# Performance work log

Measured on AMD Instinct MI355X. Metric: run time of the kernel, lower is better.

The kernel has to match this reference:

```python
import jax, jax.numpy as jnp
import numpy as np

E = 512
H = 8
DH = E // H
LN_EPS = 1e-5


def setup_inputs() -> dict:
    key = jax.random.key(0)
    ks = jax.random.split(key, 8)
    s = 1.0 / np.sqrt(E)
    return {
        "query": jax.random.normal(ks[0], (2, 2048, E), jnp.float32),
        "key_value": jax.random.normal(ks[1], (2, 4096, E), jnp.float32),
        "Wq": jax.random.normal(ks[2], (E, E), jnp.float32) * s,
        "bq": jnp.zeros((E,), jnp.float32),
        "Wk": jax.random.normal(ks[3], (E, E), jnp.float32) * s,
        "bk": jnp.zeros((E,), jnp.float32),
        "Wv": jax.random.normal(ks[4], (E, E), jnp.float32) * s,
        "bv": jnp.zeros((E,), jnp.float32),
        "Wo": jax.random.normal(ks[5], (E, E), jnp.float32) * s,
        "bo": jnp.zeros((E,), jnp.float32),
        "ln_gamma": jnp.ones((E,), jnp.float32),
        "ln_beta": jnp.zeros((E,), jnp.float32),
    }


def reference(query, key_value, Wq, bq, Wk, bk, Wv, bv, Wo, bo, ln_gamma, ln_beta):
    B, Lq, _ = query.shape
    Lk = key_value.shape[1]
    # Projections (torch Linear: x @ W.T + b)
    q = (query @ Wq.T + bq).reshape(B, Lq, H, DH)
    k = (key_value @ Wk.T + bk).reshape(B, Lk, H, DH)
    v = (key_value @ Wv.T + bv).reshape(B, Lk, H, DH)
    scale = 1.0 / np.sqrt(DH).astype(np.float32)
    scores = jnp.einsum("bqhd,bkhd->bhqk", q, k) * scale  # [B,H,Lq,Lk]
    attn = jax.nn.softmax(scores, axis=-1)
    ctx = jnp.einsum("bhqk,bkhd->bqhd", attn, v).reshape(B, Lq, E)
    attn_out = ctx @ Wo.T + bo
    # residual + LayerNorm (dropout is identity in eval)
    x = query + attn_out
    mu = jnp.mean(x, axis=-1, keepdims=True)
    var = jnp.mean(jnp.square(x - mu), axis=-1, keepdims=True)
    return (x - mu) * jax.lax.rsqrt(var + LN_EPS) * ln_gamma + ln_beta
```

## Files before the change

### kernel.cpp

```cpp
#include <hip/hip_runtime.h>
#include <hip/hip_bf16.h>

typedef __bf16 bf16;
typedef __bf16 bf16x8 __attribute__((ext_vector_type(8)));
typedef __bf16 bf16x4 __attribute__((ext_vector_type(4)));
typedef float f32x4 __attribute__((ext_vector_type(4)));

#define MFMA16(a, b, c) __builtin_amdgcn_mfma_f32_16x16x32_bf16((a), (b), (c), 0, 0, 0)

constexpr int LQ = 2048, LK = 4096, E = 512, H = 8, DH = 64;
#define QSCALE 0.1803368801111137f

#if __has_builtin(__builtin_amdgcn_exp2f)
#define EXP2(x) __builtin_amdgcn_exp2f(x)
#else
#define EXP2(x) __expf(0.6931471805599453f * (x))
#endif

__device__ __forceinline__ bf16x8 ld8(const bf16* p) { return *(const bf16x8*)p; }

__global__ __launch_bounds__(256) void cvt4_kernel(
    const float* __restrict__ w0, const float* __restrict__ w1,
    const float* __restrict__ w2, const float* __restrict__ w3,
    bf16* __restrict__ dst) {
  const float* srcs[4] = {w0, w1, w2, w3};
  const float* src = srcs[blockIdx.y];
  bf16* d = dst + (size_t)blockIdx.y * 262144;
  int i = (blockIdx.x * 256 + threadIdx.x) * 4;
  f32x4 v = *(const f32x4*)(src + i);
  bf16x4 o;
  for (int j = 0; j < 4; ++j) o[j] = (bf16)v[j];
  *(bf16x4*)(d + i) = o;
}

__global__ __launch_bounds__(256) void proj_gemm_kernel(
    const float* __restrict__ query, const float* __restrict__ kv,
    const bf16* __restrict__ Wall,
    const float* __restrict__ bq, const float* __restrict__ bk,
    const float* __restrict__ bv,
    bf16* __restrict__ qproj, bf16* __restrict__ kproj, bf16* __restrict__ vt) {
  __shared__ bf16 smA[2][128][72];
  __shared__ bf16 smB[2][128][72];
  const int tid = threadIdx.x;
  const int lane = tid & 63, wave = tid >> 6;
  const int lrow = lane & 15, quad = lane >> 4;
  const int wm = wave & 1, wn = wave >> 1;

  int x = blockIdx.x, z, mt;
  if (x < 32) { z = 0; mt = x; }
  else if (x < 96) { z = 1; mt = x - 32; }
  else { z = 2; mt = x - 96; }
  const float* A = ((z == 0) ? query : kv) + (size_t)mt * 128 * E;
  const bf16* W = Wall + (size_t)z * 262144;
  const float* bias = (z == 0) ? bq : (z == 1) ? bk : bv;
  const int n0 = blockIdx.y * 128;

  const int arow = tid >> 4, acol = tid & 15;
  const int brow = tid >> 3, bcol = tid & 7;

  f32x4 pa[8];
  bf16x8 pb[4];
#define LOAD_T(t)                                                             \
  {                                                                           \
    for (int p = 0; p < 8; ++p)                                               \
      pa[p] = *(const f32x4*)(A + (size_t)(p * 16 + arow) * E + (t) * 64 +    \
                              acol * 4);                                      \
    for (int p = 0; p < 4; ++p)                                               \
      pb[p] = ld8(W + (size_t)(n0 + p * 32 + brow) * E + (t) * 64 + bcol * 8);\
  }
#define STORE_T(bs)                                                           \
  {                                                                           \
    for (int p = 0; p < 8; ++p) {                                             \
      bf16x4 av;                                                              \
      for (int e = 0; e < 4; ++e) av[e] = (bf16)pa[p][e];                     \
      *(bf16x4*)&smA[bs][p * 16 + arow][acol * 4] = av;                       \
    }                                                                         \
    for (int p = 0; p < 4; ++p)                                               \
      *(bf16x8*)&smB[bs][p * 32 + brow][bcol * 8] = pb[p];                    \
  }

  LOAD_T(0);
  STORE_T(0);
  LOAD_T(1);
  __syncthreads();

  f32x4 acc[4][4] = {};
  for (int t = 0; t < 8; ++t) {
    const int bs = t & 1;
    bf16x8 af[2][4], bfr[2][4];
    for (int ks = 0; ks < 2; ++ks)
      for (int i = 0; i < 4; ++i)
        af[ks][i] = ld8(&smA[bs][wm * 64 + 16 * i + lrow][ks * 32 + quad * 8]);
    for (int ks = 0; ks < 2; ++ks)
      for (int c = 0; c < 4; ++c)
        bfr[ks][c] = ld8(&smB[bs][wn * 64 + 16 * c + lrow][ks * 32 + quad * 8]);
    for (int ks = 0; ks < 2; ++ks)
      for (int i = 0; i < 4; ++i)
        for (int c = 0; c < 4; ++c)
          acc[i][c] = MFMA16(af[ks][i], bfr[ks][c], acc[i][c]);
    if (t < 7) {
      STORE_T(bs ^ 1);
      if (t < 6) LOAD_T(t + 2);
    }
    __syncthreads();
  }
#undef LOAD_T
#undef STORE_T

  const float qsc = (z == 0) ? QSCALE : 1.f;
  float bvl[4];
  for (int c = 0; c < 4; ++c) bvl[c] = bias[n0 + wn * 64 + 16 * c + lrow];
  bf16* Cs = &smA[0][0][0];
  for (int i = 0; i < 4; ++i)
    for (int c = 0; c < 4; ++c)
      for (int r = 0; r < 4; ++r) {
        int row = wm * 64 + 16 * i + 4 * quad + r;
        int col = wn * 64 + 16 * c + lrow;
        bf16 val = (bf16)((acc[i][c][r] + bvl[c]) * qsc);
        if (z < 2) Cs[row * 136 + col] = val;
        else       Cs[col * 136 + row] = val;
      }
  __syncthreads();
  const int rr = tid >> 1, hh = tid & 1;
  if (z < 2) {
    bf16* Y = (z == 0) ? qproj : kproj;
    bf16* dstp = Y + (size_t)(mt * 128 + rr) * E + n0 + hh * 64;
    for (int j = 0; j < 8; ++j)
      *(bf16x8*)(dstp + j * 8) = *(bf16x8*)&Cs[rr * 136 + hh * 64 + j * 8];
  } else {
    int m0g = mt * 128, b = m0g >> 12, kk0 = m0g & 4095;
    int ng = n0 + rr, hd = ng >> 6, d = ng & 63;
    bf16* dstp = vt + ((size_t)((b * 8 + hd) * 64 + d)) * LK + kk0 + hh * 64;
    for (int j = 0; j < 8; ++j)
      *(bf16x8*)(dstp + j * 8) = *(bf16x8*)&Cs[rr * 136 + hh * 64 + j * 8];
  }
}

__global__ __launch_bounds__(256, 2) void attn_kernel(
    const bf16* __restrict__ qp, const bf16* __restrict__ kp,
    const bf16* __restrict__ vtg, bf16* __restrict__ ctx) {
  const int tid = threadIdx.x;
  const int lane = tid & 63, wave = tid >> 6;
  const int lrow = lane & 15, quad = lane >> 4;
  const int blk = blockIdx.x;
  const int qt = blk & 31, bh = blk >> 5;
  const int b = bh >> 3, h = bh & 7;
  const int wq = wave & 1, half = wave >> 1;
  const int q0 = qt * 64 + wq * 32;

  __shared__ bf16 Ks[2][2][32][72];
  __shared__ bf16 Vs[2][2][64][40];
  __shared__ bf16 Ps[4][32][40];
  __shared__ float Lr[2][2][16];

  bf16x8 qf[2][2];
  for (int g = 0; g < 2; ++g)
    for (int s = 0; s < 2; ++s)
      qf[g][s] = ld8(qp + (size_t)(b * LQ + q0 + 16 * g + lrow) * E + h * DH +
                     32 * s + quad * 8);

  float lrun[2] = {0.f, 0.f};
  f32x4 acc[2][4] = {};

  const int th = tid & 127;
  const int krow = th >> 2, kch = th & 3;
  const int vrow = th >> 1, vch = th & 1;
  const bf16* kbase =
      kp + ((size_t)(b * LK) + half * 2048 + krow) * E + h * DH + kch * 16;
  const bf16* vbase =
      vtg + ((size_t)bh * DH + vrow) * LK + half * 2048 + vch * 16;

  bf16x8 pk0 = ld8(kbase), pk1 = ld8(kbase + 8);
  bf16x8 pv0 = ld8(vbase), pv1 = ld8(vbase + 8);

  for (int it = 0; it < 64; ++it) {
    const int bs = it & 1;
    *(bf16x8*)&Ks[half][bs][krow][kch * 16] = pk0;
    *(bf16x8*)&Ks[half][bs][krow][kch * 16 + 8] = pk1;
    *(bf16x8*)&Vs[half][bs][vrow][vch * 16] = pv0;
    *(bf16x8*)&Vs[half][bs][vrow][vch * 16 + 8] = pv1;
    __syncthreads();

    if (it < 63) {
      const bf16* kn = kbase + (size_t)(it + 1) * 32 * E;
      const bf16* vn = vbase + (it + 1) * 32;
      pk0 = ld8(kn); pk1 = ld8(kn + 8);
      pv0 = ld8(vn); pv1 = ld8(vn + 8);
    }

    bf16x8 kf[2][2], vf[4];
    for (int kt = 0; kt < 2; ++kt)
      for (int sd = 0; sd < 2; ++sd)
        kf[kt][sd] = ld8(&Ks[half][bs][16 * kt + lrow][32 * sd + quad * 8]);
    for (int c = 0; c < 4; ++c)
      vf[c] = ld8(&Vs[half][bs][16 * c + lrow][quad * 8]);

    f32x4 st[2][2];
    for (int g = 0; g < 2; ++g)
      for (int kt = 0; kt < 2; ++kt) {
        st[g][kt] = (f32x4){0.f, 0.f, 0.f, 0.f};
        st[g][kt] = MFMA16(kf[kt][0], qf[g][0], st[g][kt]);
        st[g][kt] = MFMA16(kf[kt][1], qf[g][1], st[g][kt]);
      }
    for (int g = 0; g < 2; ++g)
      for (int kt = 0; kt < 2; ++kt) {
        bf16x4 pp;
        for (int r = 0; r < 4; ++r) {
          float p = EXP2(st[g][kt][r]);
          lrun[g] += p;
          pp[r] = (bf16)p;
        }
        *(bf16x4*)&Ps[wave][16 * g + lrow][16 * kt + 4 * quad] = pp;
      }
    for (int g = 0; g < 2; ++g) {
      bf16x8 pf = ld8(&Ps[wave][16 * g + lrow][quad * 8]);
      for (int c = 0; c < 4; ++c)
        acc[g][c] = MFMA16(pf, vf[c], acc[g][c]);
    }
  }

  for (int g = 0; g < 2; ++g) {
    lrun[g] += __shfl_xor(lrun[g], 16);
    lrun[g] += __shfl_xor(lrun[g], 32);
  }

  __syncthreads();
  float* F = (float*)&Ks[0][0][0][0];
  if (half == 1) {
    for (int g = 0; g < 2; ++g)
      for (int c = 0; c < 4; ++c)
        for (int r = 0; r < 4; ++r)
          F[(wq * 32 + 16 * g + 4 * quad + r) * 65 + 16 * c + lrow] =
              acc[g][c][r];
    if (lane < 16)
      for (int g = 0; g < 2; ++g) Lr[wq][g][lrow] = lrun[g];
  }
  __syncthreads();
  if (half == 0) {
    for (int g = 0; g < 2; ++g)
      for (int r = 0; r < 4; ++r) {
        float l0 = __shfl(lrun[g], 4 * quad + r);
        float l1 = Lr[wq][g][4 * quad + r];
        float inv = 1.f / (l0 + l1);
        int m = q0 + 16 * g + 4 * quad + r;
        bf16* dst = ctx + (size_t)(b * LQ + m) * E + h * DH;
        for (int c = 0; c < 4; ++c) {
          float o = acc[g][c][r] +
                    F[(wq * 32 + 16 * g + 4 * quad + r) * 65 + 16 * c + lrow];
          dst[16 * c + lrow] = (bf16)(o * inv);
        }
      }
  }
}

__global__ __launch_bounds__(512) void outln_kernel(
    const bf16* __restrict__ Cx, const bf16* __restrict__ Wo,
    const float* __restrict__ bo, const float* __restrict__ resid,
    const float* __restrict__ gamma, const float* __restrict__ beta,
    float* __restrict__ out) {
  const int tid = threadIdx.x;
  const int lane = tid & 63, wave = tid >> 6;
  const int lrow = lane & 15, quad = lane >> 4;
  const int m0 = blockIdx.x * 16;
  const int n0 = wave * 64;

  __shared__ bf16 As[16][520];
  __shared__ bf16 Wos[512][72];
  __shared__ float red1[16][8], red2[16][8];
  {
    int r = tid >> 5, ch = tid & 31;
    const bf16* src = Cx + (size_t)(m0 + r) * E + ch * 16;
    *(bf16x8*)&As[r][ch * 16] = ld8(src);
    *(bf16x8*)&As[r][ch * 16 + 8] = ld8(src + 8);
  }
  const int wr = tid >> 3, wc = tid & 7;
  bf16x8 pw[8];
  for (int p = 0; p < 8; ++p)
    pw[p] = ld8(Wo + (size_t)(p * 64 + wr) * E + wc * 8);
  __syncthreads();

  f32x4 acc[4] = {};
  for (int t = 0; t < 8; ++t) {
    for (int p = 0; p < 8; ++p)
      *(bf16x8*)&Wos[p * 64 + wr][wc * 8] = pw[p];
    __syncthreads();
    if (t < 7)
      for (int p = 0; p < 8; ++p)
        pw[p] = ld8(Wo + (size_t)(p * 64 + wr) * E + (t + 1) * 64 + wc * 8);
    for (int ks = 0; ks < 2; ++ks) {
      bf16x8 a = *(const bf16x8*)&As[lrow][t * 64 + ks * 32 + quad * 8];
      for (int c = 0; c < 4; ++c) {
        bf16x8 w = *(const bf16x8*)&Wos[n0 + 16 * c + lrow][ks * 32 + quad * 8];
        acc[c] = MFMA16(a, w, acc[c]);
      }
    }
    __syncthreads();
  }

  float s1[4] = {}, s2[4] = {};
  for (int c = 0; c < 4; ++c) {
    int n = n0 + 16 * c + lrow;
    float bb = bo[n];
    for (int r = 0; r < 4; ++r) {
      int m = 4 * quad + r;
      float xv = acc[c][r] + bb + resid[(size_t)(m0 + m) * E + n];
      acc[c][r] = xv;
      s1[r] += xv;
      s2[r] += xv * xv;
    }
  }
  for (int off = 1; off < 16; off <<= 1)
    for (int r = 0; r < 4; ++r) {
      s1[r] += __shfl_xor(s1[r], off);
      s2[r] += __shfl_xor(s2[r], off);
    }
  if (lrow == 0)
    for (int r = 0; r < 4; ++r) {
      red1[4 * quad + r][wave] = s1[r];
      red2[4 * quad + r][wave] = s2[r];
    }
  __syncthreads();
  float mu[4], rstd[4];
  for (int r = 0; r < 4; ++r) {
    int m = 4 * quad + r;
    float t1 = 0.f, t2 = 0.f;
    for (int w = 0; w < 8; ++w) { t1 += red1[m][w]; t2 += red2[m][w]; }
    float mean = t1 * (1.f / 512.f);
    float var = t2 * (1.f / 512.f) - mean * mean;
    mu[r] = mean;
    rstd[r] = rsqrtf(var + 1e-5f);
  }
  for (int c = 0; c < 4; ++c) {
    int n = n0 + 16 * c + lrow;
    float gm = gamma[n], bt = beta[n];
    for (int r = 0; r < 4; ++r) {
      int m = m0 + 4 * quad + r;
      out[(size_t)m * E + n] = (acc[c][r] - mu[r]) * rstd[r] * gm + bt;
    }
  }
}

extern "C" void kernel_launch(void* const* d_in, const int* in_sizes, int n_in,
                              void* d_out, int out_size, void* d_ws, size_t ws_size,
                              hipStream_t stream) {
  const float* query     = (const float*)d_in[0];
  const float* key_value = (const float*)d_in[1];
  const float* Wq = (const float*)d_in[2];
  const float* bq = (const float*)d_in[3];
  const float* Wk = (const float*)d_in[4];
  const float* bk = (const float*)d_in[5];
  const float* Wv = (const float*)d_in[6];
  const float* bv = (const float*)d_in[7];
  const float* Wo = (const float*)d_in[8];
  const float* bo = (const float*)d_in[9];
  const float* gamma = (const float*)d_in[10];
  const float* beta  = (const float*)d_in[11];
  float* out = (float*)d_out;

  bf16* Wb    = (bf16*)d_ws;
  bf16* Wob   = Wb + (size_t)3 * 262144;
  bf16* qproj = Wb + (size_t)4 * 262144;
  bf16* kproj = qproj + (size_t)4096 * 512;
  bf16* vt    = kproj + (size_t)8192 * 512;

  cvt4_kernel<<<dim3(256, 4), 256, 0, stream>>>(Wq, Wk, Wv, Wo, Wb);
  proj_gemm_kernel<<<dim3(160, 4), 256, 0, stream>>>(
      query, key_value, Wb, bq, bk, bv, qproj, kproj, vt);
  attn_kernel<<<512, 256, 0, stream>>>(qproj, kproj, vt, qproj );
  outln_kernel<<<256, 512, 0, stream>>>(qproj, Wob, bo, query, gamma, beta, out);
}
```

Measured before the change: 188.1 us.

## Split attention keys four ways per block, reading K/V fragments directly from global

The attention kernel now gives each of its four waves a quarter of the key sequence for a 32-query tile, doubling the grid and raising launch bounds to 4 blocks per SM. The LDS staging and per-iteration barriers for K/V are removed, and MFMA fragments are loaded straight from global/L2. Block indices are swizzled so that co-resident blocks share heads, and s_setprio is wrapped around the MFMA sections. A four-way LDS reduction merges the partial outputs and row sums. The aim is to drop barrier and LDS overhead and raise occupancy, at the cost of more uncoalesced global loads and more redundant K/V traffic across blocks.

Result: slower. 246.1 us (+30.8%).

```diff
diff --git a/kernel.cpp b/kernel.cpp
--- a/kernel.cpp
+++ b/kernel.cpp
@@ -136,22 +136,24 @@
   }
 }
 
-__global__ __launch_bounds__(256, 2) void attn_kernel(
+__global__ __launch_bounds__(256, 4) void attn_kernel(
     const bf16* __restrict__ qp, const bf16* __restrict__ kp,
     const bf16* __restrict__ vtg, bf16* __restrict__ ctx) {
   const int tid = threadIdx.x;
   const int lane = tid & 63, wave = tid >> 6;
   const int lrow = lane & 15, quad = lane >> 4;
-  const int blk = blockIdx.x;
-  const int qt = blk & 31, bh = blk >> 5;
+  const int hw = blockIdx.x;
+  const int blk = (hw & 7) * 128 + (hw >> 3);
+  const int bh = blk >> 6, qt = blk & 63;
   const int b = bh >> 3, h = bh & 7;
-  const int wq = wave & 1, half = wave >> 1;
-  const int q0 = qt * 64 + wq * 32;
-
-  __shared__ bf16 Ks[2][2][32][72];
-  __shared__ bf16 Vs[2][2][64][40];
-  __shared__ bf16 Ps[4][32][40];
-  __shared__ float Lr[2][2][16];
+  const int q0 = qt * 32;
+
+  __shared__ __align__(16) char smem[4 * 32 * 68 * 4 + 128 * 4];
+  typedef bf16 PsT[32][40];
+  PsT* Ps = (PsT*)smem;
+  typedef float FT[32][68];
+  FT* F = (FT*)smem;
+  float* Lr = (float*)(smem + 4 * 32 * 68 * 4);
 
   bf16x8 qf[2][2];
   for (int g = 0; g < 2; ++g)
@@ -162,46 +164,29 @@
   float lrun[2] = {0.f, 0.f};
   f32x4 acc[2][4] = {};
 
-  const int th = tid & 127;
-  const int krow = th >> 2, kch = th & 3;
-  const int vrow = th >> 1, vch = th & 1;
-  const bf16* kbase =
-      kp + ((size_t)(b * LK) + half * 2048 + krow) * E + h * DH + kch * 16;
-  const bf16* vbase =
-      vtg + ((size_t)bh * DH + vrow) * LK + half * 2048 + vch * 16;
-
-  bf16x8 pk0 = ld8(kbase), pk1 = ld8(kbase + 8);
-  bf16x8 pv0 = ld8(vbase), pv1 = ld8(vbase + 8);
-
-  for (int it = 0; it < 64; ++it) {
-    const int bs = it & 1;
-    *(bf16x8*)&Ks[half][bs][krow][kch * 16] = pk0;
-    *(bf16x8*)&Ks[half][bs][krow][kch * 16 + 8] = pk1;
-    *(bf16x8*)&Vs[half][bs][vrow][vch * 16] = pv0;
-    *(bf16x8*)&Vs[half][bs][vrow][vch * 16 + 8] = pv1;
-    __syncthreads();
-
-    if (it < 63) {
-      const bf16* kn = kbase + (size_t)(it + 1) * 32 * E;
-      const bf16* vn = vbase + (it + 1) * 32;
-      pk0 = ld8(kn); pk1 = ld8(kn + 8);
-      pv0 = ld8(vn); pv1 = ld8(vn + 8);
-    }
-
+  const bf16* kb =
+      kp + ((size_t)(b * LK) + wave * 1024 + lrow) * E + h * DH + quad * 8;
+  const bf16* vb =
+      vtg + ((size_t)bh * DH + lrow) * LK + wave * 1024 + quad * 8;
+
+  for (int it = 0; it < 32; ++it) {
     bf16x8 kf[2][2], vf[4];
+    const bf16* kit = kb + (size_t)(it * 32) * E;
     for (int kt = 0; kt < 2; ++kt)
       for (int sd = 0; sd < 2; ++sd)
-        kf[kt][sd] = ld8(&Ks[half][bs][16 * kt + lrow][32 * sd + quad * 8]);
-    for (int c = 0; c < 4; ++c)
-      vf[c] = ld8(&Vs[half][bs][16 * c + lrow][quad * 8]);
+        kf[kt][sd] = ld8(kit + (size_t)(16 * kt) * E + 32 * sd);
+    const bf16* vit = vb + it * 32;
+    for (int c = 0; c < 4; ++c) vf[c] = ld8(vit + (size_t)(16 * c) * LK);
 
     f32x4 st[2][2];
+    __builtin_amdgcn_s_setprio(1);
     for (int g = 0; g < 2; ++g)
       for (int kt = 0; kt < 2; ++kt) {
         st[g][kt] = (f32x4){0.f, 0.f, 0.f, 0.f};
         st[g][kt] = MFMA16(kf[kt][0], qf[g][0], st[g][kt]);
         st[g][kt] = MFMA16(kf[kt][1], qf[g][1], st[g][kt]);
       }
+    __builtin_amdgcn_s_setprio(0);
     for (int g = 0; g < 2; ++g)
       for (int kt = 0; kt < 2; ++kt) {
         bf16x4 pp;
@@ -212,44 +197,41 @@
         }
         *(bf16x4*)&Ps[wave][16 * g + lrow][16 * kt + 4 * quad] = pp;
       }
+    __builtin_amdgcn_s_setprio(1);
     for (int g = 0; g < 2; ++g) {
       bf16x8 pf = ld8(&Ps[wave][16 * g + lrow][quad * 8]);
-      for (int c = 0; c < 4; ++c)
-        acc[g][c] = MFMA16(pf, vf[c], acc[g][c]);
-    }
+      for (int c = 0; c < 4; ++c) acc[g][c] = MFMA16(pf, vf[c], acc[g][c]);
+    }
+    __builtin_amdgcn_s_setprio(0);
   }
 
   for (int g = 0; g < 2; ++g) {
     lrun[g] += __shfl_xor(lrun[g], 16);
     lrun[g] += __shfl_xor(lrun[g], 32);
   }
-
-  __syncthreads();
-  float* F = (float*)&Ks[0][0][0][0];
-  if (half == 1) {
-    for (int g = 0; g < 2; ++g)
-      for (int c = 0; c < 4; ++c)
-        for (int r = 0; r < 4; ++r)
-          F[(wq * 32 + 16 * g + 4 * quad + r) * 65 + 16 * c + lrow] =
-              acc[g][c][r];
-    if (lane < 16)
-      for (int g = 0; g < 2; ++g) Lr[wq][g][lrow] = lrun[g];
-  }
-  __syncthreads();
-  if (half == 0) {
-    for (int g = 0; g < 2; ++g)
-      for (int r = 0; r < 4; ++r) {
-        float l0 = __shfl(lrun[g], 4 * quad + r);
-        float l1 = Lr[wq][g][4 * quad + r];
-        float inv = 1.f / (l0 + l1);
-        int m = q0 + 16 * g + 4 * quad + r;
-        bf16* dst = ctx + (size_t)(b * LQ + m) * E + h * DH;
-        for (int c = 0; c < 4; ++c) {
-          float o = acc[g][c][r] +
-                    F[(wq * 32 + 16 * g + 4 * quad + r) * 65 + 16 * c + lrow];
-          dst[16 * c + lrow] = (bf16)(o * inv);
-        }
-      }
+  __syncthreads();
+  for (int g = 0; g < 2; ++g)
+    for (int c = 0; c < 4; ++c)
+      for (int r = 0; r < 4; ++r)
+        F[wave][16 * g + 4 * quad + r][16 * c + lrow] = acc[g][c][r];
+  if (lane < 16) {
+    Lr[wave * 32 + lrow] = lrun[0];
+    Lr[wave * 32 + 16 + lrow] = lrun[1];
+  }
+  __syncthreads();
+  {
+    const int q = tid >> 3, d0 = (tid & 7) * 8;
+    float ls = Lr[q] + Lr[32 + q] + Lr[64 + q] + Lr[96 + q];
+    float inv = 1.f / ls;
+    float o[8] = {0.f, 0.f, 0.f, 0.f, 0.f, 0.f, 0.f, 0.f};
+    for (int w = 0; w < 4; ++w) {
+      f32x4 x0 = *(const f32x4*)&F[w][q][d0];
+      f32x4 x1 = *(const f32x4*)&F[w][q][d0 + 4];
+      for (int j = 0; j < 4; ++j) { o[j] += x0[j]; o[4 + j] += x1[j]; }
+    }
+    bf16x8 ov;
+    for (int j = 0; j < 8; ++j) ov[j] = (bf16)(o[j] * inv);
+    *(bf16x8*)(ctx + (size_t)(b * LQ + q0 + q) * E + h * DH + d0) = ov;
   }
 }
 
@@ -366,6 +348,6 @@
   cvt4_kernel<<<dim3(256, 4), 256, 0, stream>>>(Wq, Wk, Wv, Wo, Wb);
   proj_gemm_kernel<<<dim3(160, 4), 256, 0, stream>>>(
       query, key_value, Wb, bq, bk, bv, qproj, kproj, vt);
-  attn_kernel<<<512, 256, 0, stream>>>(qproj, kproj, vt, qproj );
+  attn_kernel<<<1024, 256, 0, stream>>>(qproj, kproj, vt, qproj );
   outln_kernel<<<256, 512, 0, stream>>>(qproj, Wob, bo, query, gamma, beta, out);
 }
```
